# Optimization experiments

Measured on AMD Instinct MI355X. Metric: run time of the kernel, lower is better.

Reference implementation:

```python
import jax, jax.numpy as jnp
import numpy as np

BN_EPS = 1e-5


def _bn_relu(h, gamma, beta):
    # BatchNorm1d in training mode: normalize over (batch, length) per channel
    mean = h.mean(axis=(0, 2), keepdims=True)
    var = h.var(axis=(0, 2), keepdims=True)
    h = (h - mean) * jax.lax.rsqrt(var + BN_EPS)
    h = h * gamma[None, :, None] + beta[None, :, None]
    return jax.nn.relu(h)


def _gather(ldesc, idx):
    # ldesc: [B, D, N], idx: [B, M] -> [B, D, M]
    B, D, N = ldesc.shape
    M = idx.shape[1]
    return jnp.take_along_axis(ldesc, jnp.broadcast_to(idx[:, None, :], (B, D, M)), axis=2)


def _scatter_mean(src, idx, N):
    # per-batch scatter-mean: src [B, D, M], idx [B, M] -> [B, D, N]
    def one(s, i):
        D = s.shape[0]
        sums = jnp.zeros((D, N), s.dtype).at[:, i].add(s)
        cnts = jnp.zeros((N,), s.dtype).at[i].add(1.0)
        return sums / jnp.maximum(cnts, 1.0)[None, :]
    return jax.vmap(one)(src, idx)


def _endpoint_update(ldesc, line_enc, idx, W1, b1, g1, bt1, W2, b2):
    B, D, _ = ldesc.shape
    ld = _gather(ldesc, idx)                                   # [B, D, 2L]
    # flip endpoint pairs: neighbor endpoint of each endpoint
    neigh = ld.reshape(B, D, -1, 2)[..., ::-1].reshape(B, D, -1)
    msg = jnp.concatenate([ld, neigh, line_enc], axis=1)       # [B, 3D, 2L]
    h = jnp.einsum('oc,bcm->bom', W1, msg) + b1[None, :, None]  # Conv1d k=1
    h = _bn_relu(h, g1, bt1)
    out = jnp.einsum('oc,bcm->bom', W2, h) + b2[None, :, None]
    return out                                                  # [B, D, 2L]


def setup_inputs() -> dict:
    key = jax.random.key(0)
    ks = jax.random.split(key, 12)
    B, D, N, M = 8, 256, 8192, 8192
    inp = {
        'ldesc0': jax.random.normal(ks[0], (B, D, N), jnp.float32),
        'ldesc1': jax.random.normal(ks[1], (B, D, N), jnp.float32),
        'line_enc0': jax.random.normal(ks[2], (B, D, M), jnp.float32),
        'line_enc1': jax.random.normal(ks[3], (B, D, M), jnp.float32),
        'lines_junc_idx0': jax.random.randint(ks[4], (B, M), 0, N),
        'lines_junc_idx1': jax.random.randint(ks[5], (B, M), 0, N),
        'W1': jax.random.normal(ks[6], (2 * D, 3 * D), jnp.float32) * (1.0 / np.sqrt(3 * D)),
        'b1': jnp.zeros((2 * D,), jnp.float32),
        'g1': jnp.ones((2 * D,), jnp.float32),
        'bt1': jnp.zeros((2 * D,), jnp.float32),
        'W2': jax.random.normal(ks[7], (D, 2 * D), jnp.float32) * (1.0 / np.sqrt(2 * D)),
        'b2': jnp.zeros((D,), jnp.float32),
    }
    return inp


def reference(ldesc0, ldesc1, line_enc0, line_enc1, lines_junc_idx0, lines_junc_idx1,
              W1, b1, g1, bt1, W2, b2):
    N = ldesc0.shape[2]
    up0 = _endpoint_update(ldesc0, line_enc0, lines_junc_idx0, W1, b1, g1, bt1, W2, b2)
    up1 = _endpoint_update(ldesc1, line_enc1, lines_junc_idx1, W1, b1, g1, bt1, W2, b2)
    out0 = ldesc0 + _scatter_mean(up0, lines_junc_idx0, N)
    out1 = ldesc1 + _scatter_mean(up1, lines_junc_idx1, N)
    return (out0, out1)
```

## Files before the change

### kernel.cpp

```cpp
#include <hip/hip_runtime.h>
#include <hip/hip_bf16.h>

#define B_  8
#define D_  256
#define N_  8192
#define M_  8192
#define O1_ 512
#define K1_ 768
#define K2_ 512

typedef unsigned short u16;
typedef __attribute__((ext_vector_type(8))) short bf8;
typedef __attribute__((ext_vector_type(4))) float f4;

static __device__ __forceinline__ float bf2f(u16 u) {
    unsigned v = ((unsigned)u) << 16;
    return __uint_as_float(v);
}
static __device__ __forceinline__ u16 f2bf(float f) {
    __hip_bfloat16 h = __float2bfloat16(f);
    return *reinterpret_cast<u16*>(&h);
}
static __device__ __forceinline__ void gl_lds16(const u16* g, u16* l) {
    __builtin_amdgcn_global_load_lds((const __attribute__((address_space(1))) void*)g,
                                     (__attribute__((address_space(3))) void*)l, 16, 0, 0);
}
static __device__ __forceinline__ int swz64(int r) {
    return (((r >> 1) & 1) << 4) | (((r >> 2) & 1) << 5);
}

__global__ __launch_bounds__(256) void k_transpose_all(const float* __restrict__ s0, const float* __restrict__ s1,
                                                       const float* __restrict__ s2, const float* __restrict__ s3,
                                                       u16* __restrict__ dA, u16* __restrict__ dB) {
    __shared__ float t[32][33];
    const int z = blockIdx.z;
    const int sel = z >> 3, b = z & 7;
    const float* src = (sel == 0) ? s0 : (sel == 1) ? s1 : (sel == 2) ? s2 : s3;
    u16* dst = ((sel < 2) ? dA : dB) + (size_t)(sel & 1) * B_ * N_ * D_;
    const int c0 = blockIdx.x * 32, r0 = blockIdx.y * 32;
    const int tx = threadIdx.x, ty = threadIdx.y;
    const float* s = src + (size_t)b * D_ * N_;
    u16* d = dst + (size_t)b * N_ * D_;
#pragma unroll
    for (int i = 0; i < 4; ++i) {
        int r = r0 + ty + i * 8;
        t[ty + i * 8][tx] = s[(size_t)r * N_ + (c0 + tx)];
    }
    __syncthreads();
#pragma unroll
    for (int i = 0; i < 4; ++i) {
        int c = c0 + ty + i * 8;
        d[(size_t)c * D_ + (r0 + tx)] = f2bf(t[tx][ty + i * 8]);
    }
}

__global__ __launch_bounds__(256) void k_convert_w(const float* __restrict__ W1, const float* __restrict__ W2,
                                                   u16* __restrict__ W1b, u16* __restrict__ W2b) {
    int i = blockIdx.x * 256 + threadIdx.x;
    const int n1 = O1_ * K1_;
    const int n2 = D_ * K2_;
    if (i < n1) W1b[i] = f2bf(W1[i]);
    int j = i - n1;
    if (j >= 0 && j < n2) W2b[j] = f2bf(W2[j]);
}

#define NT1 12
__global__ __launch_bounds__(512, 2) void k_gemm1(const u16* __restrict__ W1b,
                                                  const u16* __restrict__ Tld2,
                                                  const u16* __restrict__ Tle2,
                                                  const int* __restrict__ idx0,
                                                  const int* __restrict__ idx1,
                                                  u16* __restrict__ hbuf2,
                                                  float* __restrict__ stats) {
    __shared__ u16 LA[2][2][256][32];
    __shared__ u16 LB[2][2][256][32];
    const int z  = blockIdx.z;
    const int side = z >> 3, b = z & 7;
    const u16* Tld = Tld2 + (size_t)side * B_ * N_ * D_;
    const u16* Tle = Tle2 + (size_t)side * B_ * N_ * D_;
    const int* idx = side ? idx1 : idx0;
    u16* hbuf = hbuf2 + (size_t)side * B_ * M_ * O1_;
    const int o0 = blockIdx.y * 256;
    const int m0 = blockIdx.x * 256;
    const int tid = threadIdx.x;
    const int w = tid >> 6, l = tid & 63;
    const int wr = w >> 2;
    const int wc = w & 3;

    const int srow   = tid >> 2;
    const int schunk = (tid & 3) * 16;

    int na[2], nb[2], mm[2];
    const u16* aS[2];
    int bcolu[2];
#pragma unroll
    for (int j = 0; j < 2; ++j) {
        int r = j * 128 + srow;
        int m = m0 + r;
        mm[j] = m;
        na[j] = idx[b * M_ + m];
        nb[j] = idx[b * M_ + (m ^ 1)];
        int swu = (schunk ^ swz64(r)) >> 1;
        aS[j]   = W1b + (size_t)(o0 + r) * K1_ + swu;
        bcolu[j] = swu;
    }

    int aOff[8], bOff[4];
#pragma unroll
    for (int i = 0; i < 8; ++i) {
        int r = wr * 128 + i * 16 + (l & 15);
        aOff[i] = r * 32 + ((((l >> 4) * 16) ^ swz64(r)) >> 1);
    }
#pragma unroll
    for (int j = 0; j < 4; ++j) {
        int r = wc * 64 + j * 16 + (l & 15);
        bOff[j] = r * 32 + ((((l >> 4) * 16) ^ swz64(r)) >> 1);
    }

#define STAGE_A1(kt, ks, buf)                                                        \
    {                                                                                \
        _Pragma("unroll")                                                            \
        for (int j = 0; j < 2; ++j)                                                  \
            gl_lds16(aS[j] + (kt) * 64 + (ks) * 32, &LA[buf][ks][j * 128][0] + tid * 8); \
    }
#define STAGE_B1(kt, ks, buf)                                                        \
    {                                                                                \
        const int seg = (kt) >> 2;                                                   \
        const int cb  = ((kt) & 3) * 64 + (ks) * 32;                                 \
        _Pragma("unroll")                                                            \
        for (int j = 0; j < 2; ++j) {                                                \
            const u16* s;                                                            \
            if (seg == 0)      s = Tld + (size_t)(b * N_ + na[j]) * D_ + cb + bcolu[j]; \
            else if (seg == 1) s = Tld + (size_t)(b * N_ + nb[j]) * D_ + cb + bcolu[j]; \
            else               s = Tle + (size_t)(b * M_ + mm[j]) * D_ + cb + bcolu[j]; \
            gl_lds16(s, &LB[buf][ks][j * 128][0] + tid * 8);                         \
        }                                                                            \
    }

    f4 acc[8][4];
#pragma unroll
    for (int i = 0; i < 8; ++i)
#pragma unroll
        for (int j = 0; j < 4; ++j) acc[i][j] = {0.f, 0.f, 0.f, 0.f};

    STAGE_A1(0, 0, 0); STAGE_B1(0, 0, 0);
    STAGE_A1(0, 1, 0); STAGE_B1(0, 1, 0);
    STAGE_A1(1, 0, 1); STAGE_B1(1, 0, 1);
    asm volatile("s_waitcnt vmcnt(8)" ::: "memory");
    __builtin_amdgcn_s_barrier();
    __builtin_amdgcn_sched_barrier(0);

    for (int t = 0; t < NT1; ++t) {
        const int bufp = t & 1, nbuf = bufp ^ 1;
        const u16* baseA0 = &LA[bufp][0][0][0];
        const u16* baseA1 = &LA[bufp][1][0][0];
        const u16* baseB0 = &LB[bufp][0][0][0];
        const u16* baseB1 = &LB[bufp][1][0][0];
        bf8 aF[4], bF[4];

#pragma unroll
        for (int j = 0; j < 4; ++j) bF[j] = *reinterpret_cast<const bf8*>(baseB0 + bOff[j]);
#pragma unroll
        for (int ii = 0; ii < 4; ++ii) aF[ii] = *reinterpret_cast<const bf8*>(baseA0 + aOff[ii]);
        if (t + 1 < NT1) STAGE_A1(t + 1, 1, nbuf);
        __builtin_amdgcn_s_barrier();
        asm volatile("s_waitcnt lgkmcnt(0)" ::: "memory");
        __builtin_amdgcn_sched_barrier(0);
        __builtin_amdgcn_s_setprio(1);
#pragma unroll
        for (int ii = 0; ii < 4; ++ii)
#pragma unroll
            for (int j = 0; j < 4; ++j)
                acc[ii][j] = __builtin_amdgcn_mfma_f32_16x16x32_bf16(aF[ii], bF[j], acc[ii][j], 0, 0, 0);
        __builtin_amdgcn_s_setprio(0);
        __builtin_amdgcn_s_barrier();
        __builtin_amdgcn_sched_barrier(0);

#pragma unroll
        for (int ii = 0; ii < 4; ++ii) aF[ii] = *reinterpret_cast<const bf8*>(baseA0 + aOff[4 + ii]);
        if (t + 1 < NT1) STAGE_B1(t + 1, 1, nbuf);
        __builtin_amdgcn_s_barrier();
        asm volatile("s_waitcnt lgkmcnt(0)" ::: "memory");
        __builtin_amdgcn_sched_barrier(0);
        __builtin_amdgcn_s_setprio(1);
#pragma unroll
        for (int ii = 0; ii < 4; ++ii)
#pragma unroll
            for (int j = 0; j < 4; ++j)
                acc[4 + ii][j] = __builtin_amdgcn_mfma_f32_16x16x32_bf16(aF[ii], bF[j], acc[4 + ii][j], 0, 0, 0);
        __builtin_amdgcn_s_setprio(0);
        if (t < NT1 - 2) asm volatile("s_waitcnt vmcnt(8)" ::: "memory");
        else             asm volatile("s_waitcnt vmcnt(0)" ::: "memory");
        __builtin_amdgcn_s_barrier();
        __builtin_amdgcn_sched_barrier(0);

#pragma unroll
        for (int j = 0; j < 4; ++j) bF[j] = *reinterpret_cast<const bf8*>(baseB1 + bOff[j]);
#pragma unroll
        for (int ii = 0; ii < 4; ++ii) aF[ii] = *reinterpret_cast<const bf8*>(baseA1 + aOff[ii]);
        if (t + 2 < NT1) STAGE_A1(t + 2, 0, bufp);
        __builtin_amdgcn_s_barrier();
        asm volatile("s_waitcnt lgkmcnt(0)" ::: "memory");
        __builtin_amdgcn_sched_barrier(0);
        __builtin_amdgcn_s_setprio(1);
#pragma unroll
        for (int ii = 0; ii < 4; ++ii)
#pragma unroll
            for (int j = 0; j < 4; ++j)
                acc[ii][j] = __builtin_amdgcn_mfma_f32_16x16x32_bf16(aF[ii], bF[j], acc[ii][j], 0, 0, 0);
        __builtin_amdgcn_s_setprio(0);
        __builtin_amdgcn_s_barrier();
        __builtin_amdgcn_sched_barrier(0);

#pragma unroll
        for (int ii = 0; ii < 4; ++ii) aF[ii] = *reinterpret_cast<const bf8*>(baseA1 + aOff[4 + ii]);
        if (t + 2 < NT1) STAGE_B1(t + 2, 0, bufp);
        __builtin_amdgcn_s_barrier();
        asm volatile("s_waitcnt lgkmcnt(0)" ::: "memory");
        __builtin_amdgcn_sched_barrier(0);
        __builtin_amdgcn_s_setprio(1);
#pragma unroll
        for (int ii = 0; ii < 4; ++ii)
#pragma unroll
            for (int j = 0; j < 4; ++j)
                acc[4 + ii][j] = __builtin_amdgcn_mfma_f32_16x16x32_bf16(aF[ii], bF[j], acc[4 + ii][j], 0, 0, 0);
        __builtin_amdgcn_s_setprio(0);
        if (t < NT1 - 2) asm volatile("s_waitcnt vmcnt(8)" ::: "memory");
        else             asm volatile("s_waitcnt vmcnt(0)" ::: "memory");
        __builtin_amdgcn_s_barrier();
        __builtin_amdgcn_sched_barrier(0);
    }
#undef STAGE_A1
#undef STAGE_B1

    float* redS = (float*)&LA[0][0][0][0];
    float* redQ = (float*)&LA[0][0][0][0] + 1024;
#pragma unroll
    for (int i = 0; i < 8; ++i) {
#pragma unroll
        for (int r = 0; r < 4; ++r) {
            float s = acc[i][0][r] + acc[i][1][r] + acc[i][2][r] + acc[i][3][r];
            float q = acc[i][0][r] * acc[i][0][r] + acc[i][1][r] * acc[i][1][r]
                    + acc[i][2][r] * acc[i][2][r] + acc[i][3][r] * acc[i][3][r];
#pragma unroll
            for (int mk = 1; mk < 16; mk <<= 1) {
                s += __shfl_xor(s, mk, 16);
                q += __shfl_xor(q, mk, 16);
            }
            if ((l & 15) == 0) {
                int ch = wr * 128 + i * 16 + (l >> 4) * 4 + r;
                redS[ch * 4 + wc] = s;
                redQ[ch * 4 + wc] = q;
            }
        }
    }
    __syncthreads();
    if (tid < 256) {
        float s = redS[tid * 4] + redS[tid * 4 + 1] + redS[tid * 4 + 2] + redS[tid * 4 + 3];
        float q = redQ[tid * 4] + redQ[tid * 4 + 1] + redQ[tid * 4 + 2] + redQ[tid * 4 + 3];
        atomicAdd(&stats[side * 1024 + o0 + tid], s);
        atomicAdd(&stats[side * 1024 + 512 + o0 + tid], q);
    }

#pragma unroll
    for (int j = 0; j < 4; ++j) {
        int m = m0 + wc * 64 + j * 16 + (l & 15);
        size_t rowbase = (size_t)(b * M_ + m) * O1_;
#pragma unroll
        for (int i = 0; i < 8; ++i) {
            int orow = o0 + wr * 128 + i * 16 + (l >> 4) * 4;
            ushort4 pk;
            pk.x = f2bf(acc[i][j].x);
            pk.y = f2bf(acc[i][j].y);
            pk.z = f2bf(acc[i][j].z);
            pk.w = f2bf(acc[i][j].w);
            *reinterpret_cast<ushort4*>(&hbuf[rowbase + orow]) = pk;
        }
    }
}

__global__ void k_finalize_ac(const float* __restrict__ stats, const float* __restrict__ g1,
                              const float* __restrict__ bt1, float* __restrict__ ac) {
    int i = blockIdx.x * 256 + threadIdx.x;
    if (i >= 1024) return;
    int side = i >> 9, o = i & 511;
    const float* st = stats + side * 1024;
    const float inv = 1.0f / ((float)B_ * (float)M_);
    float mean = st[o] * inv;
    float var  = st[O1_ + o] * inv - mean * mean;
    var = fmaxf(var, 0.0f);
    float a = g1[o] * rsqrtf(var + 1e-5f);
    ac[side * 1024 + o] = a;
    ac[side * 1024 + O1_ + o] = bt1[o] - mean * a;
}

__global__ void k_count_int(const int* __restrict__ idx0, const int* __restrict__ idx1, int* __restrict__ cnt2) {
    int i = blockIdx.x * 256 + threadIdx.x;
    if (i < 2 * B_ * M_) {
        int side = i >> 16, j = i & 65535;
        const int* idx = side ? idx1 : idx0;
        atomicAdd(&cnt2[side * B_ * N_ + (j >> 13) * N_ + idx[j]], 1);
    }
}

__global__ __launch_bounds__(1024) void k_scan(const int* __restrict__ cnt2, int* __restrict__ offs2,
                                               int* __restrict__ fill2) {
    __shared__ int wsum[1024];
    const int base = blockIdx.x * N_;
    const int t = threadIdx.x;
    int v[8]; int s = 0;
#pragma unroll
    for (int k = 0; k < 8; ++k) { v[k] = cnt2[base + t * 8 + k]; s += v[k]; }
    wsum[t] = s;
    __syncthreads();
    for (int off = 1; off < 1024; off <<= 1) {
        int add = (t >= off) ? wsum[t - off] : 0;
        __syncthreads();
        wsum[t] += add;
        __syncthreads();
    }
    int run = (t > 0) ? wsum[t - 1] : 0;
#pragma unroll
    for (int k = 0; k < 8; ++k) {
        offs2[base + t * 8 + k] = run;
        fill2[base + t * 8 + k] = run;
        run += v[k];
    }
}

__global__ void k_fill(const int* __restrict__ idx0, const int* __restrict__ idx1,
                       int* __restrict__ fill2, int* __restrict__ mlist2) {
    int i = blockIdx.x * 256 + threadIdx.x;
    if (i < 2 * B_ * M_) {
        int side = i >> 16, j = i & 65535;
        const int* idx = side ? idx1 : idx0;
        int b = j >> 13, m = j & (M_ - 1);
        int pos = atomicAdd(&fill2[side * B_ * N_ + b * N_ + idx[j]], 1);
        mlist2[(size_t)side * B_ * M_ + b * M_ + pos] = m;
    }
}

__global__ __launch_bounds__(512) void k_gemm2(const u16* __restrict__ W2b,
                                               const u16* __restrict__ hbuf2,
                                               const float* __restrict__ ac,
                                               const float* __restrict__ b2,
                                               u16* __restrict__ up2) {
    __shared__ u16 At[256 * 32];
    __shared__ u16 Bt[128 * 32];
    __shared__ float acs[1024];
    __shared__ float bcs[256];
    const int z = blockIdx.z;
    const int side = z >> 3, b = z & 7;
    const u16* hbuf = hbuf2 + (size_t)side * B_ * M_ * O1_;
    u16* up = up2 + (size_t)side * B_ * M_ * D_;
    const float* acp = ac + side * 1024;
    const int m0 = blockIdx.x * 128;
    const int tid = threadIdx.x;
    const int w = tid >> 6, l = tid & 63;
    const int wr = w >> 2;
    const int wc = w & 3;

    acs[tid]       = acp[tid];
    acs[tid + 512] = acp[tid + 512];
    if (tid < 256) bcs[tid] = b2[tid];

    const int srow   = tid >> 2;
    const int schunk = (tid & 3) * 16;
    const int lcu    = (tid & 3) * 8;

    const u16* aS[2];
#pragma unroll
    for (int j = 0; j < 2; ++j) {
        int r = j * 128 + srow;
        aS[j] = W2b + (size_t)r * K2_ + ((schunk ^ swz64(r)) >> 1);
    }
    const u16* pB = hbuf + (size_t)(b * M_ + m0 + srow) * O1_ + lcu;
    u16* bDst = &Bt[srow * 32 + ((schunk ^ swz64(srow)) >> 1)];

    int aOff[8], bOff[2];
#pragma unroll
    for (int i = 0; i < 8; ++i) {
        int r = wr * 128 + i * 16 + (l & 15);
        aOff[i] = r * 32 + ((((l >> 4) * 16) ^ swz64(r)) >> 1);
    }
#pragma unroll
    for (int j = 0; j < 2; ++j) {
        int r = wc * 32 + j * 16 + (l & 15);
        bOff[j] = r * 32 + ((((l >> 4) * 16) ^ swz64(r)) >> 1);
    }

    f4 acc[8][2];
#pragma unroll
    for (int i = 0; i < 8; ++i)
#pragma unroll
        for (int j = 0; j < 2; ++j) acc[i][j] = {0.f, 0.f, 0.f, 0.f};

    __syncthreads();

    for (int kk = 0; kk < 16; ++kk) {
        const int o = kk * 32 + lcu;
        f4 A0 = *reinterpret_cast<const f4*>(&acs[o]);
        f4 A1 = *reinterpret_cast<const f4*>(&acs[o + 4]);
        f4 C0 = *reinterpret_cast<const f4*>(&acs[512 + o]);
        f4 C1 = *reinterpret_cast<const f4*>(&acs[512 + o + 4]);
#pragma unroll
        for (int j = 0; j < 2; ++j)
            gl_lds16(aS[j] + kk * 32, At + j * 128 * 32 + tid * 8);
        {
            const ushort4* ps = reinterpret_cast<const ushort4*>(pB + kk * 32);
            ushort4 v0 = ps[0], v1 = ps[1];
            union { ushort4 u4[2]; bf8 v8; } pk;
            pk.u4[0].x = f2bf(fmaxf(bf2f(v0.x) * A0.x + C0.x, 0.0f));
            pk.u4[0].y = f2bf(fmaxf(bf2f(v0.y) * A0.y + C0.y, 0.0f));
            pk.u4[0].z = f2bf(fmaxf(bf2f(v0.z) * A0.z + C0.z, 0.0f));
            pk.u4[0].w = f2bf(fmaxf(bf2f(v0.w) * A0.w + C0.w, 0.0f));
            pk.u4[1].x = f2bf(fmaxf(bf2f(v1.x) * A1.x + C1.x, 0.0f));
            pk.u4[1].y = f2bf(fmaxf(bf2f(v1.y) * A1.y + C1.y, 0.0f));
            pk.u4[1].z = f2bf(fmaxf(bf2f(v1.z) * A1.z + C1.z, 0.0f));
            pk.u4[1].w = f2bf(fmaxf(bf2f(v1.w) * A1.w + C1.w, 0.0f));
            *reinterpret_cast<bf8*>(bDst) = pk.v8;
        }
        __syncthreads();
        bf8 aF[8], bF[2];
#pragma unroll
        for (int i = 0; i < 8; ++i) aF[i] = *reinterpret_cast<const bf8*>(&At[aOff[i]]);
#pragma unroll
        for (int j = 0; j < 2; ++j) bF[j] = *reinterpret_cast<const bf8*>(&Bt[bOff[j]]);
#pragma unroll
        for (int i = 0; i < 8; ++i)
#pragma unroll
            for (int j = 0; j < 2; ++j)
                acc[i][j] = __builtin_amdgcn_mfma_f32_16x16x32_bf16(aF[i], bF[j], acc[i][j], 0, 0, 0);
        __syncthreads();
    }

#pragma unroll
    for (int j = 0; j < 2; ++j) {
        int m = m0 + wc * 32 + j * 16 + (l & 15);
        size_t rowbase = (size_t)(b * M_ + m) * D_;
#pragma unroll
        for (int i = 0; i < 8; ++i) {
            int d = wr * 128 + i * 16 + (l >> 4) * 4;
            ushort4 pk;
            pk.x = f2bf(acc[i][j].x + bcs[d + 0]);
            pk.y = f2bf(acc[i][j].y + bcs[d + 1]);
            pk.z = f2bf(acc[i][j].z + bcs[d + 2]);
            pk.w = f2bf(acc[i][j].w + bcs[d + 3]);
            *reinterpret_cast<ushort4*>(&up[rowbase + d]) = pk;
        }
    }
}

__global__ __launch_bounds__(256) void k_reduce_finalize(const float* __restrict__ ldesc0,
                                                         const float* __restrict__ ldesc1,
                                                         const u16* __restrict__ up2,
                                                         const int* __restrict__ cnt2,
                                                         const int* __restrict__ offs2,
                                                         const int* __restrict__ mlist2,
                                                         float* __restrict__ out) {
    __shared__ float lds[32][257];
    const int z = blockIdx.z;
    const int side = z >> 3, b = z & 7;
    const float* ldesc = side ? ldesc1 : ldesc0;
    const u16* up = up2 + (size_t)side * B_ * M_ * D_;
    const int* cnt  = cnt2  + side * B_ * N_;
    const int* offs = offs2 + side * B_ * N_;
    const int* mlist = mlist2 + (size_t)side * B_ * M_;
    float* outp = out + (size_t)side * B_ * D_ * N_;
    const int n0 = blockIdx.x * 32;
    const int tx = threadIdx.x, ty = threadIdx.y;
#pragma unroll
    for (int i = 0; i < 4; ++i) {
        int nl = ty + i * 8;
        int n  = n0 + nl;
        int c   = cnt[b * N_ + n];
        int off = offs[b * N_ + n];
        float inv = 1.0f / (float)max(c, 1);
        float acc[8] = {0.f, 0.f, 0.f, 0.f, 0.f, 0.f, 0.f, 0.f};
        for (int e = 0; e < c; ++e) {
            int m = mlist[(size_t)b * M_ + off + e];
            const ushort4* row = reinterpret_cast<const ushort4*>(up + (size_t)(b * M_ + m) * D_ + tx * 8);
            ushort4 aa = row[0], bb = row[1];
            acc[0] += bf2f(aa.x); acc[1] += bf2f(aa.y); acc[2] += bf2f(aa.z); acc[3] += bf2f(aa.w);
            acc[4] += bf2f(bb.x); acc[5] += bf2f(bb.y); acc[6] += bf2f(bb.z); acc[7] += bf2f(bb.w);
        }
#pragma unroll
        for (int k = 0; k < 8; ++k) lds[nl][tx * 8 + k] = acc[k] * inv;
    }
    __syncthreads();
#pragma unroll
    for (int i = 0; i < 32; ++i) {
        int d = ty + i * 8;
        size_t o2 = (size_t)(b * D_ + d) * N_ + n0 + tx;
        outp[o2] = ldesc[o2] + lds[tx][d];
    }
}

__global__ void k_marker(float* out, float v) { out[0] = v; }

extern "C" void kernel_launch(void* const* d_in, const int* in_sizes, int n_in,
                              void* d_out, int out_size, void* d_ws, size_t ws_size,
                              hipStream_t stream) {
    const float* ldesc0 = (const float*)d_in[0];
    const float* ldesc1 = (const float*)d_in[1];
    const float* le0    = (const float*)d_in[2];
    const float* le1    = (const float*)d_in[3];
    const int*   idx0   = (const int*)d_in[4];
    const int*   idx1   = (const int*)d_in[5];
    const float* W1     = (const float*)d_in[6];
    const float* g1     = (const float*)d_in[8];
    const float* bt1    = (const float*)d_in[9];
    const float* W2     = (const float*)d_in[10];
    const float* b2     = (const float*)d_in[11];
    float* out = (float*)d_out;

    char* ws = (char*)d_ws;
    const size_t SIDE_BND = (size_t)B_ * N_ * D_ * 2;
    const size_t oTld2  = 0;
    const size_t oTle2  = 2 * SIDE_BND;
    const size_t oH2    = 4 * SIDE_BND;
    const size_t oW1b   = oH2 + (size_t)2 * B_ * M_ * O1_ * 2;
    const size_t oW2b   = oW1b + 786432;
    const size_t oStats = oW2b + 262144;
    const size_t oAC    = oStats + 8192;
    const size_t NEED   = oAC + 8192;
    if (ws_size < NEED) {
        k_marker<<<1, 1, 0, stream>>>(out, 1000.0f + (float)(ws_size >> 20));
        return;
    }
    u16*   Tld2  = (u16*)(ws + oTld2);
    u16*   up2   = (u16*)(ws + oTld2);
    u16*   Tle2  = (u16*)(ws + oTle2);
    int*   cnt2  = (int*)(ws + oTle2);
    int*   offs2 = (int*)(ws + oTle2 + 524288);
    int*   fill2 = (int*)(ws + oTle2 + 1048576);
    int*   mlist2= (int*)(ws + oTle2 + 1572864);
    u16*   hbuf2 = (u16*)(ws + oH2);
    u16*   W1b   = (u16*)(ws + oW1b);
    u16*   W2b   = (u16*)(ws + oW2b);
    float* stats = (float*)(ws + oStats);
    float* ac    = (float*)(ws + oAC);

    k_convert_w<<<2048, 256, 0, stream>>>(W1, W2, W1b, W2b);

    const dim3 tb(32, 8);
    k_transpose_all<<<dim3(N_ / 32, D_ / 32, 32), tb, 0, stream>>>(ldesc0, ldesc1, le0, le1, Tld2, Tle2);
    hipMemsetAsync(stats, 0, 8192, stream);
    k_gemm1<<<dim3(M_ / 256, O1_ / 256, 16), 512, 0, stream>>>(W1b, Tld2, Tle2, idx0, idx1, hbuf2, stats);
    k_finalize_ac<<<4, 256, 0, stream>>>(stats, g1, bt1, ac);
    hipMemsetAsync(cnt2, 0, (size_t)2 * B_ * N_ * 4, stream);
    k_count_int<<<2 * B_ * M_ / 256, 256, 0, stream>>>(idx0, idx1, cnt2);
    k_scan<<<16, 1024, 0, stream>>>(cnt2, offs2, fill2);
    k_fill<<<2 * B_ * M_ / 256, 256, 0, stream>>>(idx0, idx1, fill2, mlist2);
    k_gemm2<<<dim3(M_ / 128, 1, 16), 512, 0, stream>>>(W2b, hbuf2, ac, b2, up2);
    k_reduce_finalize<<<dim3(N_ / 32, 1, 16), tb, 0, stream>>>(ldesc0, ldesc1, up2, cnt2, offs2, mlist2, out);
}
```

Before: 413.6 us.

## Split BN statistics into separate kernel and take residual from bf16 transposed ldesc

Moves the per-channel sum and sum-of-squares reduction out of the first GEMM epilogue into a standalone k_stats kernel that re-reads the bf16 hidden buffer. The final reduce kernel now adds the residual from the transposed bf16 copy of ldesc instead of re-reading the fp32 input. That needs a separate buffer for the update tensor so the transposed copy survives. The aim is a lighter GEMM epilogue and less residual read traffic, at the cost of an extra full pass over the hidden buffer. The output residual and the BN statistics now carry bf16 rounding error.

```diff
diff --git a/kernel.cpp b/kernel.cpp
--- a/kernel.cpp
+++ b/kernel.cpp
@@ -70,8 +70,7 @@
                                                   const u16* __restrict__ Tle2,
                                                   const int* __restrict__ idx0,
                                                   const int* __restrict__ idx1,
-                                                  u16* __restrict__ hbuf2,
-                                                  float* __restrict__ stats) {
+                                                  u16* __restrict__ hbuf2) {
     __shared__ u16 LA[2][2][256][32];
     __shared__ u16 LB[2][2][256][32];
     const int z  = blockIdx.z;
@@ -233,35 +232,6 @@
 #undef STAGE_A1
 #undef STAGE_B1
 
-    float* redS = (float*)&LA[0][0][0][0];
-    float* redQ = (float*)&LA[0][0][0][0] + 1024;
-#pragma unroll
-    for (int i = 0; i < 8; ++i) {
-#pragma unroll
-        for (int r = 0; r < 4; ++r) {
-            float s = acc[i][0][r] + acc[i][1][r] + acc[i][2][r] + acc[i][3][r];
-            float q = acc[i][0][r] * acc[i][0][r] + acc[i][1][r] * acc[i][1][r]
-                    + acc[i][2][r] * acc[i][2][r] + acc[i][3][r] * acc[i][3][r];
-#pragma unroll
-            for (int mk = 1; mk < 16; mk <<= 1) {
-                s += __shfl_xor(s, mk, 16);
-                q += __shfl_xor(q, mk, 16);
-            }
-            if ((l & 15) == 0) {
-                int ch = wr * 128 + i * 16 + (l >> 4) * 4 + r;
-                redS[ch * 4 + wc] = s;
-                redQ[ch * 4 + wc] = q;
-            }
-        }
-    }
-    __syncthreads();
-    if (tid < 256) {
-        float s = redS[tid * 4] + redS[tid * 4 + 1] + redS[tid * 4 + 2] + redS[tid * 4 + 3];
-        float q = redQ[tid * 4] + redQ[tid * 4 + 1] + redQ[tid * 4 + 2] + redQ[tid * 4 + 3];
-        atomicAdd(&stats[side * 1024 + o0 + tid], s);
-        atomicAdd(&stats[side * 1024 + 512 + o0 + tid], q);
-    }
-
 #pragma unroll
     for (int j = 0; j < 4; ++j) {
         int m = m0 + wc * 64 + j * 16 + (l & 15);
@@ -277,6 +247,27 @@
             *reinterpret_cast<ushort4*>(&hbuf[rowbase + orow]) = pk;
         }
     }
+}
+
+__global__ __launch_bounds__(256) void k_stats(const u16* __restrict__ hbuf2, float* __restrict__ stats) {
+    const int side = blockIdx.x >> 8;
+    const int blk  = blockIdx.x & 255;
+    const u16* hb = hbuf2 + (size_t)side * B_ * M_ * O1_;
+    float* st = stats + side * 1024;
+    const int t = threadIdx.x;
+    const size_t row0 = (size_t)blk * 256;
+    float s0 = 0.f, q0 = 0.f, s1 = 0.f, q1 = 0.f;
+    for (int r = 0; r < 256; ++r) {
+        const u16* p = hb + (row0 + r) * O1_;
+        float v0 = bf2f(p[t]);
+        float v1 = bf2f(p[t + 256]);
+        s0 += v0; q0 += v0 * v0;
+        s1 += v1; q1 += v1 * v1;
+    }
+    atomicAdd(&st[t], s0);
+    atomicAdd(&st[O1_ + t], q0);
+    atomicAdd(&st[t + 256], s1);
+    atomicAdd(&st[O1_ + t + 256], q1);
 }
 
 __global__ void k_finalize_ac(const float* __restrict__ stats, const float* __restrict__ g1,
@@ -451,8 +442,7 @@
     }
 }
 
-__global__ __launch_bounds__(256) void k_reduce_finalize(const float* __restrict__ ldesc0,
-                                                         const float* __restrict__ ldesc1,
+__global__ __launch_bounds__(256) void k_reduce_finalize(const u16* __restrict__ Tld2,
                                                          const u16* __restrict__ up2,
                                                          const int* __restrict__ cnt2,
                                                          const int* __restrict__ offs2,
@@ -461,7 +451,7 @@
     __shared__ float lds[32][257];
     const int z = blockIdx.z;
     const int side = z >> 3, b = z & 7;
-    const float* ldesc = side ? ldesc1 : ldesc0;
+    const u16* tld = Tld2 + (size_t)side * B_ * N_ * D_;
     const u16* up = up2 + (size_t)side * B_ * M_ * D_;
     const int* cnt  = cnt2  + side * B_ * N_;
     const int* offs = offs2 + side * B_ * N_;
@@ -484,15 +474,23 @@
             acc[0] += bf2f(aa.x); acc[1] += bf2f(aa.y); acc[2] += bf2f(aa.z); acc[3] += bf2f(aa.w);
             acc[4] += bf2f(bb.x); acc[5] += bf2f(bb.y); acc[6] += bf2f(bb.z); acc[7] += bf2f(bb.w);
         }
-#pragma unroll
-        for (int k = 0; k < 8; ++k) lds[nl][tx * 8 + k] = acc[k] * inv;
+        const ushort4* lrow = reinterpret_cast<const ushort4*>(tld + (size_t)(b * N_ + n) * D_ + tx * 8);
+        ushort4 la = lrow[0], lb = lrow[1];
+        lds[nl][tx * 8 + 0] = acc[0] * inv + bf2f(la.x);
+        lds[nl][tx * 8 + 1] = acc[1] * inv + bf2f(la.y);
+        lds[nl][tx * 8 + 2] = acc[2] * inv + bf2f(la.z);
+        lds[nl][tx * 8 + 3] = acc[3] * inv + bf2f(la.w);
+        lds[nl][tx * 8 + 4] = acc[4] * inv + bf2f(lb.x);
+        lds[nl][tx * 8 + 5] = acc[5] * inv + bf2f(lb.y);
+        lds[nl][tx * 8 + 6] = acc[6] * inv + bf2f(lb.z);
+        lds[nl][tx * 8 + 7] = acc[7] * inv + bf2f(lb.w);
     }
     __syncthreads();
 #pragma unroll
     for (int i = 0; i < 32; ++i) {
         int d = ty + i * 8;
         size_t o2 = (size_t)(b * D_ + d) * N_ + n0 + tx;
-        outp[o2] = ldesc[o2] + lds[tx][d];
+        outp[o2] = lds[tx][d];
     }
 }
 
@@ -519,7 +517,8 @@
     const size_t oTld2  = 0;
     const size_t oTle2  = 2 * SIDE_BND;
     const size_t oH2    = 4 * SIDE_BND;
-    const size_t oW1b   = oH2 + (size_t)2 * B_ * M_ * O1_ * 2;
+    const size_t oUp2   = oH2 + (size_t)2 * B_ * M_ * O1_ * 2;
+    const size_t oW1b   = oUp2 + 2 * SIDE_BND;
     const size_t oW2b   = oW1b + 786432;
     const size_t oStats = oW2b + 262144;
     const size_t oAC    = oStats + 8192;
@@ -529,13 +528,13 @@
         return;
     }
     u16*   Tld2  = (u16*)(ws + oTld2);
-    u16*   up2   = (u16*)(ws + oTld2);
     u16*   Tle2  = (u16*)(ws + oTle2);
     int*   cnt2  = (int*)(ws + oTle2);
     int*   offs2 = (int*)(ws + oTle2 + 524288);
     int*   fill2 = (int*)(ws + oTle2 + 1048576);
     int*   mlist2= (int*)(ws + oTle2 + 1572864);
     u16*   hbuf2 = (u16*)(ws + oH2);
+    u16*   up2   = (u16*)(ws + oUp2);
     u16*   W1b   = (u16*)(ws + oW1b);
     u16*   W2b   = (u16*)(ws + oW2b);
     float* stats = (float*)(ws + oStats);
@@ -545,13 +544,14 @@
 
     const dim3 tb(32, 8);
     k_transpose_all<<<dim3(N_ / 32, D_ / 32, 32), tb, 0, stream>>>(ldesc0, ldesc1, le0, le1, Tld2, Tle2);
+    k_gemm1<<<dim3(M_ / 256, O1_ / 256, 16), 512, 0, stream>>>(W1b, Tld2, Tle2, idx0, idx1, hbuf2);
     hipMemsetAsync(stats, 0, 8192, stream);
-    k_gemm1<<<dim3(M_ / 256, O1_ / 256, 16), 512, 0, stream>>>(W1b, Tld2, Tle2, idx0, idx1, hbuf2, stats);
+    k_stats<<<512, 256, 0, stream>>>(hbuf2, stats);
     k_finalize_ac<<<4, 256, 0, stream>>>(stats, g1, bt1, ac);
     hipMemsetAsync(cnt2, 0, (size_t)2 * B_ * N_ * 4, stream);
     k_count_int<<<2 * B_ * M_ / 256, 256, 0, stream>>>(idx0, idx1, cnt2);
     k_scan<<<16, 1024, 0, stream>>>(cnt2, offs2, fill2);
     k_fill<<<2 * B_ * M_ / 256, 256, 0, stream>>>(idx0, idx1, fill2, mlist2);
     k_gemm2<<<dim3(M_ / 128, 1, 16), 512, 0, stream>>>(W2b, hbuf2, ac, b2, up2);
-    k_reduce_finalize<<<dim3(N_ / 32, 1, 16), tb, 0, stream>>>(ldesc0, ldesc1, up2, cnt2, offs2, mlist2, out);
-}
+    k_reduce_finalize<<<dim3(N_ / 32, 1, 16), tb, 0, stream>>>(Tld2, up2, cnt2, offs2, mlist2, out);
+}
```

Measured after the change: 416.2 us. Within noise of the previous version (+0.6%).
